# Kernel optimization log

Measured on AMD Instinct MI355X. Metric: run time of the kernel, lower is better.

The kernel has to match this reference:

```python
import jax, jax.numpy as jnp
import numpy as np

T, B, OBS, H, ACT = 256, 1024, 256, 256, 64
SLOPE = 0.1


def setup_inputs() -> dict:
    key = jax.random.key(0)
    ks = jax.random.split(key, 20)
    stdv = 1.0 / np.sqrt(H)
    u = lambda k, shape: jax.random.uniform(k, shape, jnp.float32, -stdv, stdv)
    return {
        "x": jax.random.normal(ks[0], (T, B, OBS), jnp.float32),
        "noise1": jax.random.uniform(ks[1], (T, B, 1), jnp.float32),
        "noise2": jax.random.uniform(ks[2], (T, B, 1), jnp.float32),
        # FCEncoder: two Linear+ReLU layers
        "We1": u(ks[3], (OBS, H)), "be1": u(ks[4], (H,)),
        "We2": u(ks[5], (H, H)), "be2": u(ks[6], (H,)),
        # cell_1 (bottom): U_11 [bottom,4H+1], U_21 [top,4H+1], W_01 [H,4H+1], bias
        "U11_1": u(ks[7], (H, 4 * H + 1)), "U21_1": u(ks[8], (H, 4 * H + 1)),
        "W01_1": u(ks[9], (H, 4 * H + 1)), "b1": u(ks[10], (4 * H + 1,)),
        # cell_2 (top, last layer): no U_21
        "U11_2": u(ks[11], (H, 4 * H + 1)), "W01_2": u(ks[12], (H, 4 * H + 1)),
        "b2": u(ks[13], (4 * H + 1,)),
        "Wh": u(ks[14], (H, H)), "bh": u(ks[15], (H,)),
        "Wp": u(ks[16], (H, ACT)), "bp": u(ks[17], (ACT,)),
    }


def _trigger_train(z_hat, noise):
    # forward: (noise < z_hat).float(); backward: 0.1 * identity (straight-through)
    hard = (noise < z_hat).astype(z_hat.dtype)
    return jax.lax.stop_gradient(hard) + 0.1 * (z_hat - jax.lax.stop_gradient(z_hat))


def _gates(f_s):
    f = jax.nn.sigmoid(f_s[:, 0:H])
    i = jax.nn.sigmoid(f_s[:, H:2 * H])
    o = jax.nn.sigmoid(f_s[:, 2 * H:3 * H])
    g = jnp.tanh(f_s[:, 3 * H:4 * H])
    z_hat = jnp.clip((SLOPE * f_s[:, 4 * H:4 * H + 1] + 1.0) / 2.0, 0.05, 0.95)
    return f, i, o, g, z_hat


def reference(x, noise1, noise2, We1, be1, We2, be2,
              U11_1, U21_1, W01_1, b1, U11_2, W01_2, b2, Wh, bh, Wp, bp):
    # encoder over all timesteps at once (parallel_wrapper equivalent)
    xe = jax.nn.relu(jnp.einsum('tbi,ih->tbh', x, We1) + be1)
    xe = jax.nn.relu(jnp.einsum('tbi,ih->tbh', xe, We2) + be2)

    def step(carry, inp):
        h1, c1, z1, h2, c2 = carry
        xt, n1, n2 = inp
        # ---- cell 1 (not last layer; z_bottom = 1) ----
        fs1 = h1 @ W01_1 + z1 * (h2 @ U21_1) + xt @ U11_1 + b1
        f, i, o, g, zhat1 = _gates(fs1)
        c1n = f * c1 + i * g              # z_bottom == 1 everywhere
        h1n = o * jnp.tanh(c1n)
        z1n = _trigger_train(zhat1, n1)
        # ---- cell 2 (last layer; z_bottom = z1n, s_topdown = 0) ----
        fs2 = h2 @ W01_2 + z1n * (h1n @ U11_2) + b2
        f2, i2, o2, g2, zhat2 = _gates(fs2)
        c2n = (1.0 - z1n) * c2 + z1n * (f2 * c2 + i2 * g2)
        h2n = o2 * jnp.tanh(c2n)
        _ = _trigger_train(zhat2, n2)
        return (h1n, c1n, z1n, h2n, c2n), h2n

    zeros = jnp.zeros((B, H), jnp.float32)
    init = (zeros, zeros, jnp.ones((B, 1), jnp.float32), zeros, zeros)
    _, emb = jax.lax.scan(step, init, (xe, noise1, noise2))  # emb: [T,B,H]

    hid = jax.nn.relu(jnp.einsum('tbh,hk->tbk', emb, Wh) + bh)
    pred = jnp.tanh(jnp.einsum('tbh,ha->tba', hid, Wp) + bp)
    return pred
```

## Files before the change

### kernel.cpp

```cpp
#include <hip/hip_runtime.h>
#include <math.h>

typedef __attribute__((ext_vector_type(8))) _Float16 half8;
typedef __attribute__((ext_vector_type(4))) float    f32x4;
typedef unsigned long long u64;

#define NSTEP 256
#define CH    32
#define NCHUNK (NSTEP/CH)
#define NB    1024
#define HID   256
#define BH    262144
#define LK    40
#define LK1   776
#define LW2   520
#define INV2K 4.8828125e-4f

#define W1H_OFF 0
#define W1L_OFF 49664
#define W2H_OFF 99328
#define WZ_OFF  132608
#define PAN_OFF 135680
#define SEQ_SMEM 135936

__device__ __forceinline__ float sigf(float x){ return 1.f/(1.f+expf(-x)); }
__device__ __forceinline__ void splitf(float v, _Float16& h, _Float16& l){
    h = (_Float16)v; l = (_Float16)((v - (float)h)*2048.f);
}

__global__ __launch_bounds__(256)
void wsplit_k(const float* __restrict__ s0, const float* __restrict__ s1,
              const float* __restrict__ s2, int K, int N, int ldn,
              int kb1, int kb2, int perm,
              _Float16* __restrict__ oh, _Float16* __restrict__ ol)
{
    int idx = blockIdx.x*256 + threadIdx.x;
    if (idx >= N*K) return;
    int n = idx / K, k = idx - n*K;
    int jsrc = perm ? ((n&3)*256 + (n>>2)) : n;
    const float* s = (k < kb1) ? &s0[(size_t)k*ldn]
                   : (k < kb2) ? &s1[(size_t)(k-kb1)*ldn]
                               : &s2[(size_t)(k-kb2)*ldn];
    float v = s[jsrc];
    _Float16 h, l; splitf(v, h, l);
    oh[idx] = h; ol[idx] = l;
}

__global__ void wz_k(const float* __restrict__ W01, const float* __restrict__ U21,
                     const float* __restrict__ U11, float* __restrict__ wz)
{
    int k = blockIdx.x*256 + threadIdx.x;
    if (k >= 768) return;
    wz[k] = (k < 256) ? W01[(size_t)k*1025 + 1024]
          : (k < 512) ? U21[(size_t)(k-256)*1025 + 1024]
                      : U11[(size_t)(k-512)*1025 + 1024];
}

__global__ __launch_bounds__(256)
void init_k(_Float16* h1H, _Float16* h1L, _Float16* h2H, _Float16* h2L,
            float* c1g, float* c2g, unsigned* zcb)
{
    int i = blockIdx.x*256 + threadIdx.x;
    h1H[i] = (_Float16)0.f; h1L[i] = (_Float16)0.f;
    h2H[i] = (_Float16)0.f; h2L[i] = (_Float16)0.f;
    c1g[i] = 0.f; c2g[i] = 0.f;
    if (i < NB) zcb[i] = 1u;
}

template<int AIN, int AOUT, int NCOL>
__global__ __launch_bounds__(256)
void gemm_t(const float* __restrict__ Af,
            const _Float16* __restrict__ Ah_, const _Float16* __restrict__ Al_,
            const _Float16* __restrict__ Bh_, const _Float16* __restrict__ Bl_,
            const float* __restrict__ bias,
            _Float16* __restrict__ Oh, _Float16* __restrict__ Ol,
            float* __restrict__ Of)
{
    constexpr int NT = 8;
    __shared__ __align__(16) char smem[40960];

    const int tid  = threadIdx.x;
    const size_t R0 = (size_t)blockIdx.x*64;
    const int C0   = blockIdx.y*64;
    const int rh   = (tid>>6)&1, ch = tid>>7;
    const int lane = tid&63, lr = lane&15, kq = (lane>>4)<<3;
    const int arow = tid>>2, seg = tid&3;
    const size_t abase = (R0+arow)*256 + seg*8;
    const size_t wbase = (size_t)(C0 + (tid>>2))*256 + seg*8;

    f32x4 am[2][2], ax[2][2];
#pragma unroll
    for (int r=0;r<2;++r)
#pragma unroll
        for (int c=0;c<2;++c){ am[r][c]=(f32x4)0.f; ax[r][c]=(f32x4)0.f; }

    half8 rah, ral, rwh, rwl;
    auto load_tile = [&](int k0, half8& ah, half8& al, half8& wh, half8& wl) {
        if (AIN == 0) {
            float4 a0 = *(const float4*)(Af + abase + k0);
            float4 a1 = *(const float4*)(Af + abase + k0 + 4);
            float av[8] = {a0.x,a0.y,a0.z,a0.w,a1.x,a1.y,a1.z,a1.w};
#pragma unroll
            for (int i=0;i<8;++i){ _Float16 h,l; splitf(av[i],h,l); ah[i]=h; al[i]=l; }
        } else {
            ah = *(const half8*)(Ah_ + abase + k0);
            al = *(const half8*)(Al_ + abase + k0);
        }
        wh = *(const half8*)(Bh_ + wbase + k0);
        wl = *(const half8*)(Bl_ + wbase + k0);
    };
    auto store_tile = [&](int buf) {
        char* bs = smem + buf*20480;
        *(half8*)((_Float16*)(bs        ) + arow*LK + seg*8) = rah;
        *(half8*)((_Float16*)(bs +  5120) + arow*LK + seg*8) = ral;
        *(half8*)((_Float16*)(bs + 10240) + (tid>>2)*LK + seg*8) = rwh;
        *(half8*)((_Float16*)(bs + 15360) + (tid>>2)*LK + seg*8) = rwl;
    };

    load_tile(0, rah, ral, rwh, rwl);
    store_tile(0);

#pragma unroll 2
    for (int kb = 0; kb < NT; ++kb) {
        const int buf = kb & 1;
        half8 nah, nal, nwh, nwl;
        if (kb+1 < NT) load_tile((kb+1)*32, nah, nal, nwh, nwl);
        __syncthreads();
        const char* bs = smem + buf*20480;
        const _Float16* LAh = (const _Float16*)bs;
        const _Float16* LAl = (const _Float16*)(bs +  5120);
        const _Float16* LBh = (const _Float16*)(bs + 10240);
        const _Float16* LBl = (const _Float16*)(bs + 15360);
        half8 fah[2], fal[2], fbh[2], fbl[2];
#pragma unroll
        for (int rf=0;rf<2;++rf) {
            fah[rf] = *(const half8*)(LAh + (rh*32+rf*16+lr)*LK + kq);
            fal[rf] = *(const half8*)(LAl + (rh*32+rf*16+lr)*LK + kq);
        }
#pragma unroll
        for (int cf=0;cf<2;++cf) {
            fbh[cf] = *(const half8*)(LBh + (ch*32+cf*16+lr)*LK + kq);
            fbl[cf] = *(const half8*)(LBl + (ch*32+cf*16+lr)*LK + kq);
        }
#pragma unroll
        for (int cf=0;cf<2;++cf)
#pragma unroll
            for (int rf=0;rf<2;++rf) {
                am[rf][cf] = __builtin_amdgcn_mfma_f32_16x16x32_f16(fah[rf], fbh[cf], am[rf][cf],0,0,0);
                ax[rf][cf] = __builtin_amdgcn_mfma_f32_16x16x32_f16(fah[rf], fbl[cf], ax[rf][cf],0,0,0);
                ax[rf][cf] = __builtin_amdgcn_mfma_f32_16x16x32_f16(fal[rf], fbh[cf], ax[rf][cf],0,0,0);
            }
        if (kb+1 < NT) {
            rah=nah; ral=nal; rwh=nwh; rwl=nwl;
            store_tile((kb+1)&1);
        }
    }

#pragma unroll
    for (int cf=0;cf<2;++cf) {
        int col = C0 + ch*32 + cf*16 + lr;
        float bcol = bias[col];
#pragma unroll
        for (int rf=0;rf<2;++rf)
#pragma unroll
            for (int q=0;q<4;++q) {
                size_t row = R0 + rh*32 + rf*16 + ((lane>>4)<<2) + q;
                float v = am[rf][cf][q] + ax[rf][cf][q]*INV2K + bcol;
                if (AOUT == 0) {
                    v = fmaxf(v, 0.f);
                    _Float16 h,l; splitf(v,h,l);
                    Oh[row*NCOL + col] = h;
                    Ol[row*NCOL + col] = l;
                } else {
                    Of[row*NCOL + col] = tanhf(v);
                }
            }
    }
}

struct PArgs {
    const _Float16 *XeH, *XeL;
    _Float16 *EmH, *EmL;
    const _Float16 *W1h, *W1l, *W2h, *W2l;
    const float *b1, *b2, *wz, *noise;
    _Float16 *h1rH, *h1rL, *h2rH, *h2rL;
    unsigned *zcb;
    float *c1g, *c2g;
    unsigned *ctr;
    unsigned *tick;
    int chunk;
};

__device__ __forceinline__ void barrier_arrive(unsigned* c, int tid)
{
    __syncthreads();
    if (tid == 0)
        __hip_atomic_fetch_add(c, 1u, __ATOMIC_RELAXED, __HIP_MEMORY_SCOPE_AGENT);
}
__device__ __forceinline__ void barrier_wait(unsigned* c, int tid)
{
    if (tid == 0) {
        int guard = 0;
        while (__hip_atomic_load(c, __ATOMIC_RELAXED, __HIP_MEMORY_SCOPE_AGENT) < 32u
               && guard < (1<<17)) {
            __builtin_amdgcn_s_sleep(1);
            ++guard;
        }
    }
    __syncthreads();
}

__global__ __launch_bounds__(512, 1)
void hm_pers_k(PArgs a)
{
    extern __shared__ __align__(16) char smem[];

    const int tid = threadIdx.x, wv = tid>>6, lane = tid&63;
    const int lr = lane&15, hq = lane>>4, kg8 = hq<<3;

    unsigned* pan_sh = (unsigned*)(smem + PAN_OFF);
    if (tid == 0) {
        unsigned xcc;
        asm volatile("s_getreg_b32 %0, hwreg(HW_REG_XCC_ID)" : "=s"(xcc));
        xcc &= 7u;
        unsigned slot = __hip_atomic_fetch_add(a.tick + a.chunk*8 + xcc, 1u,
                          __ATOMIC_RELAXED, __HIP_MEMORY_SCOPE_AGENT);
        pan_sh[0] = xcc;
        pan_sh[1] = slot & 31u;
    }
    __syncthreads();
    const int panel = pan_sh[0], cs = pan_sh[1];
    const int R0 = panel*128, hb = cs*8;
    const int row = R0 + wv*16 + lr;
    const size_t rbase = (size_t)row*HID;
    const int hc0 = hb + hq, hc1 = hb + 4 + hq;

    float b1v[2][4], b2v[2][4];
#pragma unroll
    for (int cf=0; cf<2; ++cf)
#pragma unroll
        for (int q=0;q<4;++q) {
            int hc = hb + cf*4 + hq;
            b1v[cf][q] = a.b1[q*256 + hc];
            b2v[cf][q] = a.b2[q*256 + hc];
        }
    const float b1z = a.b1[1024];

#pragma unroll
    for (int it = 0; it < 12; ++it) {
        int idx = it*512 + tid;
        int hl  = idx >= 3072;
        int e   = idx - hl*3072;
        int c   = e / 96;
        int ks  = e - c*96;
        const _Float16* src = (hl ? a.W1l : a.W1h)
            + (size_t)(cs*32 + c)*768 + ks*8;
        *(half8*)(smem + (hl ? W1L_OFF : W1H_OFF) + (c*LK1 + ks*8)*2)
            = *(const half8*)src;
    }
#pragma unroll
    for (int it = 0; it < 4; ++it) {
        int idx = it*512 + tid;
        int c   = idx >> 6;
        int ks  = idx & 63;
        const _Float16* src = a.W2h + (size_t)(cs*32 + c)*512 + ks*8;
        *(half8*)(smem + W2H_OFF + (c*LW2 + ks*8)*2) = *(const half8*)src;
    }
    {
        float* wzl = (float*)(smem + WZ_OFF);
        for (int i = tid; i < 768; i += 512) wzl[i] = a.wz[i];
    }
    __syncthreads();
    const float* wzl = (const float*)(smem + WZ_OFF);

    float c1s[2] = { a.c1g[rbase + hc0], a.c1g[rbase + hc1] };
    float c2s[2] = { a.c2g[rbase + hc0], a.c2g[rbase + hc1] };
    bool zrv = a.zcb[row] != 0u;

    const _Float16* w2lp[2] = {
        a.W2l + (size_t)(cs*32      + lr)*512 + kg8,
        a.W2l + (size_t)(cs*32 + 16 + lr)*512 + kg8
    };

    half8 pf_h[4], pf_l[4];
    half8 xf_h[8], xf_l[8];
    {
        const _Float16* xeh0 = a.XeH + (size_t)(a.chunk*CH)*BH;
        const _Float16* xel0 = a.XeL + (size_t)(a.chunk*CH)*BH;
#pragma unroll
        for (int kt = 0; kt < 4; ++kt) {
            pf_h[kt] = *(const half8*)(a.h1rH + rbase + kt*32 + kg8);
            pf_l[kt] = *(const half8*)(a.h1rL + rbase + kt*32 + kg8);
        }
#pragma unroll
        for (int j = 0; j < 8; ++j) {
            xf_h[j] = *(const half8*)(xeh0 + rbase + j*32 + kg8);
            xf_l[j] = *(const half8*)(xel0 + rbase + j*32 + kg8);
        }
    }

#pragma unroll 1
    for (int s = 0; s < CH; ++s) {
        const int t = a.chunk*CH + s;
        const _Float16* h1cH = a.h1rH + (size_t)s*BH;
        const _Float16* h1cL = a.h1rL + (size_t)s*BH;
        _Float16*       h1nH = a.h1rH + (size_t)(s+1)*BH;
        _Float16*       h1nL = a.h1rL + (size_t)(s+1)*BH;
        const _Float16* h2cH = a.h2rH + (size_t)s*BH;
        const _Float16* h2cL = a.h2rL + (size_t)s*BH;
        _Float16*       h2nH = a.h2rH + (size_t)(s+1)*BH;
        _Float16*       h2nL = a.h2rL + (size_t)(s+1)*BH;

        auto ld1 = [&](int kt, half8& h, half8& l){
            const int k0 = kt*32;
            if (k0 < 256) { h = *(const half8*)(h1cH + rbase + k0 + kg8);
                            l = *(const half8*)(h1cL + rbase + k0 + kg8); }
            else          { h = *(const half8*)(h2cH + rbase + (k0-256) + kg8);
                            l = *(const half8*)(h2cL + rbase + (k0-256) + kg8); }
        };
        auto ld2 = [&](int kt, half8& h, half8& l){
            const int k0 = kt*32;
            if (k0 < 256) { h = *(const half8*)(h2cH + rbase + k0 + kg8);
                            l = *(const half8*)(h2cL + rbase + k0 + kg8); }
            else          { h = *(const half8*)(h1nH + rbase + (k0-256) + kg8);
                            l = *(const half8*)(h1nL + rbase + (k0-256) + kg8); }
        };

        f32x4 am[2], ax[2];
        am[0]=(f32x4)0.f; am[1]=(f32x4)0.f; ax[0]=(f32x4)0.f; ax[1]=(f32x4)0.f;
        float zacc = 0.f;

#pragma unroll
        for (int kt = 0; kt < 24; ++kt) {
            half8 sh, sl;
            if (kt < 16) { sh = pf_h[kt&3]; sl = pf_l[kt&3]; }
            else         { sh = xf_h[kt-16]; sl = xf_l[kt-16]; }
            if (kt+4 < 16) ld1(kt+4, pf_h[kt&3], pf_l[kt&3]);
            if (kt >= 8 && kt < 16 && !zrv) { sh = half8{}; sl = half8{}; }
#pragma unroll
            for (int i = 0; i < 8; ++i)
                zacc = fmaf((float)sh[i] + (float)sl[i]*INV2K,
                            wzl[kt*32 + kg8 + i], zacc);
#pragma unroll
            for (int cf = 0; cf < 2; ++cf) {
                const int wb = (cf*16 + lr)*LK1 + kt*32 + kg8;
                half8 wh = *(const half8*)((const _Float16*)(smem + W1H_OFF) + wb);
                half8 wl = *(const half8*)((const _Float16*)(smem + W1L_OFF) + wb);
                am[cf] = __builtin_amdgcn_mfma_f32_16x16x32_f16(wh, sh, am[cf],0,0,0);
                ax[cf] = __builtin_amdgcn_mfma_f32_16x16x32_f16(wl, sh, ax[cf],0,0,0);
                ax[cf] = __builtin_amdgcn_mfma_f32_16x16x32_f16(wh, sl, ax[cf],0,0,0);
            }
        }
        zacc += __shfl_xor(zacc, 16);
        zacc += __shfl_xor(zacc, 32);

        float fsz = zacc + b1z;
        float zh = fminf(fmaxf((0.1f*fsz + 1.f)*0.5f, 0.05f), 0.95f);
        const bool znv = a.noise[(size_t)t*NB + row] < zh;

#pragma unroll
        for (int cf = 0; cf < 2; ++cf) {
            float v0 = am[cf][0] + ax[cf][0]*INV2K + b1v[cf][0];
            float v1 = am[cf][1] + ax[cf][1]*INV2K + b1v[cf][1];
            float v2 = am[cf][2] + ax[cf][2]*INV2K + b1v[cf][2];
            float v3 = am[cf][3] + ax[cf][3]*INV2K + b1v[cf][3];
            float f = sigf(v0), i = sigf(v1), o = sigf(v2), g = tanhf(v3);
            float cn = f*c1s[cf] + i*g;
            c1s[cf] = cn;
            float hn = o*tanhf(cn);
            _Float16 hh, hl; splitf(hn, hh, hl);
            const int hc = (cf==0) ? hc0 : hc1;
            h1nH[rbase + hc] = hh; h1nL[rbase + hc] = hl;
            if (s == CH-1) { a.h1rH[rbase + hc] = hh; a.h1rL[rbase + hc] = hl; }
        }
        if (s == CH-1 && hq == 0) a.zcb[row] = znv ? 1u : 0u;

        unsigned* b1c = a.ctr + ((size_t)(a.chunk*CH + s)*2 + 0)*8 + panel;
        barrier_arrive(b1c, tid);

        am[0]=(f32x4)0.f; am[1]=(f32x4)0.f; ax[0]=(f32x4)0.f; ax[1]=(f32x4)0.f;
#pragma unroll
        for (int kt = 0; kt < 4; ++kt) ld2(kt, pf_h[kt], pf_l[kt]);
#pragma unroll
        for (int kt = 0; kt < 8; ++kt) {
            half8 sh = pf_h[kt&3], sl = pf_l[kt&3];
            if (kt+4 < 8) ld2(kt+4, pf_h[kt&3], pf_l[kt&3]);
#pragma unroll
            for (int cf = 0; cf < 2; ++cf) {
                const int wb = (cf*16 + lr)*LW2 + kt*32 + kg8;
                half8 wh = *(const half8*)((const _Float16*)(smem + W2H_OFF) + wb);
                half8 wl = *(const half8*)(w2lp[cf] + kt*32);
                am[cf] = __builtin_amdgcn_mfma_f32_16x16x32_f16(wh, sh, am[cf],0,0,0);
                ax[cf] = __builtin_amdgcn_mfma_f32_16x16x32_f16(wl, sh, ax[cf],0,0,0);
                ax[cf] = __builtin_amdgcn_mfma_f32_16x16x32_f16(wh, sl, ax[cf],0,0,0);
            }
        }
        barrier_wait(b1c, tid);

#pragma unroll
        for (int kt = 8; kt < 12; ++kt) ld2(kt, pf_h[kt&3], pf_l[kt&3]);
#pragma unroll
        for (int kt = 8; kt < 16; ++kt) {
            half8 sh = pf_h[kt&3], sl = pf_l[kt&3];
            if (kt+4 < 16) ld2(kt+4, pf_h[kt&3], pf_l[kt&3]);
            if (!znv) { sh = half8{}; sl = half8{}; }
#pragma unroll
            for (int cf = 0; cf < 2; ++cf) {
                const int wb = (cf*16 + lr)*LW2 + kt*32 + kg8;
                half8 wh = *(const half8*)((const _Float16*)(smem + W2H_OFF) + wb);
                half8 wl = *(const half8*)(w2lp[cf] + kt*32);
                am[cf] = __builtin_amdgcn_mfma_f32_16x16x32_f16(wh, sh, am[cf],0,0,0);
                ax[cf] = __builtin_amdgcn_mfma_f32_16x16x32_f16(wl, sh, ax[cf],0,0,0);
                ax[cf] = __builtin_amdgcn_mfma_f32_16x16x32_f16(wh, sl, ax[cf],0,0,0);
            }
        }

#pragma unroll
        for (int cf = 0; cf < 2; ++cf) {
            float v0 = am[cf][0] + ax[cf][0]*INV2K + b2v[cf][0];
            float v1 = am[cf][1] + ax[cf][1]*INV2K + b2v[cf][1];
            float v2 = am[cf][2] + ax[cf][2]*INV2K + b2v[cf][2];
            float v3 = am[cf][3] + ax[cf][3]*INV2K + b2v[cf][3];
            float f = sigf(v0), i = sigf(v1), o = sigf(v2), g = tanhf(v3);
            float cn = znv ? (f*c2s[cf] + i*g) : c2s[cf];
            c2s[cf] = cn;
            float hn = o*tanhf(cn);
            _Float16 hh, hl; splitf(hn, hh, hl);
            const int hc = (cf==0) ? hc0 : hc1;
            h2nH[rbase + hc] = hh; h2nL[rbase + hc] = hl;
            a.EmH[(size_t)t*BH + rbase + hc] = hh;
            a.EmL[(size_t)t*BH + rbase + hc] = hl;
            if (s == CH-1) { a.h2rH[rbase + hc] = hh; a.h2rL[rbase + hc] = hl; }
        }
        zrv = znv;

        unsigned* b2c = a.ctr + ((size_t)(a.chunk*CH + s)*2 + 1)*8 + panel;
        barrier_arrive(b2c, tid);
        if (s+1 < CH) {
            const _Float16* xehn = a.XeH + (size_t)(t+1)*BH;
            const _Float16* xeln = a.XeL + (size_t)(t+1)*BH;
#pragma unroll
            for (int kt = 0; kt < 4; ++kt) {
                pf_h[kt] = *(const half8*)(h1nH + rbase + kt*32 + kg8);
                pf_l[kt] = *(const half8*)(h1nL + rbase + kt*32 + kg8);
            }
#pragma unroll
            for (int j = 0; j < 8; ++j) {
                xf_h[j] = *(const half8*)(xehn + rbase + j*32 + kg8);
                xf_l[j] = *(const half8*)(xeln + rbase + j*32 + kg8);
            }
        }
        barrier_wait(b2c, tid);
    }

    a.c1g[rbase + hc0] = c1s[0]; a.c1g[rbase + hc1] = c1s[1];
    a.c2g[rbase + hc0] = c2s[0]; a.c2g[rbase + hc1] = c2s[1];
}

extern "C" void kernel_launch(void* const* d_in, const int* in_sizes, int n_in,
                              void* d_out, int out_size, void* d_ws, size_t ws_size,
                              hipStream_t stream)
{
    const float* x     = (const float*)d_in[0];
    const float* n1    = (const float*)d_in[1];
    const float* We1   = (const float*)d_in[3];
    const float* be1   = (const float*)d_in[4];
    const float* We2   = (const float*)d_in[5];
    const float* be2   = (const float*)d_in[6];
    const float* U11_1 = (const float*)d_in[7];
    const float* U21_1 = (const float*)d_in[8];
    const float* W01_1 = (const float*)d_in[9];
    const float* b1    = (const float*)d_in[10];
    const float* U11_2 = (const float*)d_in[11];
    const float* W01_2 = (const float*)d_in[12];
    const float* b2    = (const float*)d_in[13];
    const float* Wh    = (const float*)d_in[14];
    const float* bh    = (const float*)d_in[15];
    const float* Wp    = (const float*)d_in[16];
    const float* bp_   = (const float*)d_in[17];
    float* out = (float*)d_out;

    char* p = (char*)d_ws;
    auto alloc = [&](size_t bytes){ char* q = p; p += (bytes + 255) & ~(size_t)255; return q; };
    _Float16* XeH  = (_Float16*)alloc((size_t)NSTEP*BH*2);
    _Float16* XeL  = (_Float16*)alloc((size_t)NSTEP*BH*2);
    _Float16* EmH  = (_Float16*)alloc((size_t)NSTEP*BH*2);
    _Float16* EmL  = (_Float16*)alloc((size_t)NSTEP*BH*2);
    _Float16* Wt1h = (_Float16*)alloc((size_t)1024*768*2);
    _Float16* Wt1l = (_Float16*)alloc((size_t)1024*768*2);
    _Float16* Wt2h = (_Float16*)alloc((size_t)1024*512*2);
    _Float16* Wt2l = (_Float16*)alloc((size_t)1024*512*2);
    _Float16* We1h = (_Float16*)alloc(256*256*2);
    _Float16* We1l = (_Float16*)alloc(256*256*2);
    _Float16* We2h = (_Float16*)alloc(256*256*2);
    _Float16* We2l = (_Float16*)alloc(256*256*2);
    _Float16* Whh  = (_Float16*)alloc(256*256*2);
    _Float16* Whl  = (_Float16*)alloc(256*256*2);
    _Float16* Wph  = (_Float16*)alloc(64*256*2);
    _Float16* Wpl  = (_Float16*)alloc(64*256*2);
    float*    wz1  = (float*)alloc(768*4);
    _Float16* h1rH = (_Float16*)alloc((size_t)(CH+1)*BH*2);
    _Float16* h1rL = (_Float16*)alloc((size_t)(CH+1)*BH*2);
    _Float16* h2rH = (_Float16*)alloc((size_t)(CH+1)*BH*2);
    _Float16* h2rL = (_Float16*)alloc((size_t)(CH+1)*BH*2);
    unsigned* zcb  = (unsigned*)alloc(NB*4);
    float*    c1g  = (float*)alloc((size_t)BH*4);
    float*    c2g  = (float*)alloc((size_t)BH*4);
    unsigned* ctr  = (unsigned*)alloc((size_t)NCHUNK*CH*2*8*4);
    unsigned* tick = (unsigned*)alloc((size_t)NCHUNK*8*4);
    if (ws_size < (size_t)(p - (char*)d_ws)) return;

    _Float16* TmpH = EmH; _Float16* TmpL = EmL;
    _Float16* TpH  = XeH; _Float16* TpL  = XeL;

    wsplit_k<<<dim3(3072), 256, 0, stream>>>(W01_1, U21_1, U11_1, 768, 1024, 1025, 256, 512, 1, Wt1h, Wt1l);
    wsplit_k<<<dim3(2048), 256, 0, stream>>>(W01_2, U11_2, nullptr, 512, 1024, 1025, 256, 512, 1, Wt2h, Wt2l);
    wsplit_k<<<dim3(256),  256, 0, stream>>>(We1, nullptr, nullptr, 256, 256, 256, 256, 256, 0, We1h, We1l);
    wsplit_k<<<dim3(256),  256, 0, stream>>>(We2, nullptr, nullptr, 256, 256, 256, 256, 256, 0, We2h, We2l);
    wsplit_k<<<dim3(256),  256, 0, stream>>>(Wh,  nullptr, nullptr, 256, 256, 256, 256, 256, 0, Whh,  Whl);
    wsplit_k<<<dim3(64),   256, 0, stream>>>(Wp,  nullptr, nullptr, 256, 64, 64, 256, 256, 0, Wph, Wpl);
    wz_k<<<dim3(3), 256, 0, stream>>>(W01_1, U21_1, U11_1, wz1);
    init_k<<<dim3(1024), 256, 0, stream>>>(h1rH, h1rL, h2rH, h2rL, c1g, c2g, zcb);
    (void)hipMemsetAsync(ctr, 0, (size_t)NCHUNK*CH*2*8*4, stream);
    (void)hipMemsetAsync(tick, 0, (size_t)NCHUNK*8*4, stream);

    for (int c = 0; c < 8; ++c) {
        size_t ro = (size_t)c*32*BH;
        gemm_t<0,0,256><<<dim3(512,4), 256, 0, stream>>>(
            x + ro, nullptr, nullptr, We1h, We1l, be1, TmpH, TmpL, nullptr);
        gemm_t<1,0,256><<<dim3(512,4), 256, 0, stream>>>(
            nullptr, TmpH, TmpL, We2h, We2l, be2, XeH + ro, XeL + ro, nullptr);
    }

    (void)hipFuncSetAttribute((const void*)hm_pers_k,
        hipFuncAttributeMaxDynamicSharedMemorySize, SEQ_SMEM);
    PArgs pa;
    pa.XeH = XeH; pa.XeL = XeL; pa.EmH = EmH; pa.EmL = EmL;
    pa.W1h = Wt1h; pa.W1l = Wt1l; pa.W2h = Wt2h; pa.W2l = Wt2l;
    pa.b1 = b1; pa.b2 = b2; pa.wz = wz1; pa.noise = n1;
    pa.h1rH = h1rH; pa.h1rL = h1rL; pa.h2rH = h2rH; pa.h2rL = h2rL;
    pa.zcb = zcb; pa.c1g = c1g; pa.c2g = c2g; pa.ctr = ctr; pa.tick = tick;
    for (int c = 0; c < NCHUNK; ++c) {
        pa.chunk = c;
        void* kargs[] = { (void*)&pa };
        (void)hipLaunchCooperativeKernel((const void*)hm_pers_k, dim3(256), dim3(512),
                                         kargs, SEQ_SMEM, stream);
    }

    for (int c = 0; c < 8; ++c) {
        size_t ro = (size_t)c*32*BH;
        gemm_t<1,0,256><<<dim3(512,4), 256, 0, stream>>>(
            nullptr, EmH + ro, EmL + ro, Whh, Whl, bh, TpH, TpL, nullptr);
        gemm_t<1,1,64><<<dim3(512,1), 256, 0, stream>>>(
            nullptr, TpH, TpL, Wph, Wpl, bp_, nullptr, nullptr,
            out + (size_t)c*32*NB*64);
    }
}
```

Before: 8.432 ms.

## Overlap cell-1 h1 contribution before the step barrier wait in persistent recurrence

Measured after the change: 8.221 ms. -2.5%, faster.

```diff
diff --git a/kernel.cpp b/kernel.cpp
--- a/kernel.cpp
+++ b/kernel.cpp
@@ -207,7 +207,9 @@
             ++guard;
         }
     }
-    __syncthreads();
+    asm volatile("" ::: "memory");
+    __builtin_amdgcn_s_barrier();
+    asm volatile("" ::: "memory");
 }
 
 __global__ __launch_bounds__(512, 1)
@@ -284,14 +286,40 @@
 
     half8 pf_h[4], pf_l[4];
     half8 xf_h[8], xf_l[8];
+    f32x4 am1[2], ax1[2];
+    float zacc;
+
     {
-        const _Float16* xeh0 = a.XeH + (size_t)(a.chunk*CH)*BH;
-        const _Float16* xel0 = a.XeL + (size_t)(a.chunk*CH)*BH;
+        am1[0]=(f32x4)0.f; am1[1]=(f32x4)0.f;
+        ax1[0]=(f32x4)0.f; ax1[1]=(f32x4)0.f; zacc = 0.f;
 #pragma unroll
         for (int kt = 0; kt < 4; ++kt) {
             pf_h[kt] = *(const half8*)(a.h1rH + rbase + kt*32 + kg8);
             pf_l[kt] = *(const half8*)(a.h1rL + rbase + kt*32 + kg8);
         }
+#pragma unroll
+        for (int kt = 0; kt < 8; ++kt) {
+            half8 sh = pf_h[kt&3], sl = pf_l[kt&3];
+            if (kt+4 < 8) {
+                pf_h[kt&3] = *(const half8*)(a.h1rH + rbase + (kt+4)*32 + kg8);
+                pf_l[kt&3] = *(const half8*)(a.h1rL + rbase + (kt+4)*32 + kg8);
+            }
+#pragma unroll
+            for (int i = 0; i < 8; ++i)
+                zacc = fmaf((float)sh[i] + (float)sl[i]*INV2K,
+                            wzl[kt*32 + kg8 + i], zacc);
+#pragma unroll
+            for (int cf = 0; cf < 2; ++cf) {
+                const int wb = (cf*16 + lr)*LK1 + kt*32 + kg8;
+                half8 wh = *(const half8*)((const _Float16*)(smem + W1H_OFF) + wb);
+                half8 wl = *(const half8*)((const _Float16*)(smem + W1L_OFF) + wb);
+                am1[cf] = __builtin_amdgcn_mfma_f32_16x16x32_f16(wh, sh, am1[cf],0,0,0);
+                ax1[cf] = __builtin_amdgcn_mfma_f32_16x16x32_f16(wl, sh, ax1[cf],0,0,0);
+                ax1[cf] = __builtin_amdgcn_mfma_f32_16x16x32_f16(wh, sl, ax1[cf],0,0,0);
+            }
+        }
+        const _Float16* xeh0 = a.XeH + (size_t)(a.chunk*CH)*BH;
+        const _Float16* xel0 = a.XeL + (size_t)(a.chunk*CH)*BH;
 #pragma unroll
         for (int j = 0; j < 8; ++j) {
             xf_h[j] = *(const half8*)(xeh0 + rbase + j*32 + kg8);
@@ -311,12 +339,10 @@
         _Float16*       h2nH = a.h2rH + (size_t)(s+1)*BH;
         _Float16*       h2nL = a.h2rL + (size_t)(s+1)*BH;
 
-        auto ld1 = [&](int kt, half8& h, half8& l){
+        auto ld1b = [&](int kt, half8& h, half8& l){
             const int k0 = kt*32;
-            if (k0 < 256) { h = *(const half8*)(h1cH + rbase + k0 + kg8);
-                            l = *(const half8*)(h1cL + rbase + k0 + kg8); }
-            else          { h = *(const half8*)(h2cH + rbase + (k0-256) + kg8);
-                            l = *(const half8*)(h2cL + rbase + (k0-256) + kg8); }
+            h = *(const half8*)(h2cH + rbase + (k0-256) + kg8);
+            l = *(const half8*)(h2cL + rbase + (k0-256) + kg8);
         };
         auto ld2 = [&](int kt, half8& h, half8& l){
             const int k0 = kt*32;
@@ -326,17 +352,21 @@
                             l = *(const half8*)(h1nL + rbase + (k0-256) + kg8); }
         };
 
-        f32x4 am[2], ax[2];
-        am[0]=(f32x4)0.f; am[1]=(f32x4)0.f; ax[0]=(f32x4)0.f; ax[1]=(f32x4)0.f;
-        float zacc = 0.f;
-
-#pragma unroll
-        for (int kt = 0; kt < 24; ++kt) {
+        if (s > 0)
+            barrier_wait(a.ctr + ((size_t)(a.chunk*CH + s-1)*2 + 1)*8 + panel, tid);
+
+#pragma unroll
+        for (int kt = 8; kt < 12; ++kt) ld1b(kt, pf_h[kt&3], pf_l[kt&3]);
+#pragma unroll
+        for (int kt = 8; kt < 24; ++kt) {
             half8 sh, sl;
-            if (kt < 16) { sh = pf_h[kt&3]; sl = pf_l[kt&3]; }
-            else         { sh = xf_h[kt-16]; sl = xf_l[kt-16]; }
-            if (kt+4 < 16) ld1(kt+4, pf_h[kt&3], pf_l[kt&3]);
-            if (kt >= 8 && kt < 16 && !zrv) { sh = half8{}; sl = half8{}; }
+            if (kt < 16) {
+                sh = pf_h[kt&3]; sl = pf_l[kt&3];
+                if (kt+4 < 16) ld1b(kt+4, pf_h[kt&3], pf_l[kt&3]);
+                if (!zrv) { sh = half8{}; sl = half8{}; }
+            } else {
+                sh = xf_h[kt-16]; sl = xf_l[kt-16];
+            }
 #pragma unroll
             for (int i = 0; i < 8; ++i)
                 zacc = fmaf((float)sh[i] + (float)sl[i]*INV2K,
@@ -346,9 +376,9 @@
                 const int wb = (cf*16 + lr)*LK1 + kt*32 + kg8;
                 half8 wh = *(const half8*)((const _Float16*)(smem + W1H_OFF) + wb);
                 half8 wl = *(const half8*)((const _Float16*)(smem + W1L_OFF) + wb);
-                am[cf] = __builtin_amdgcn_mfma_f32_16x16x32_f16(wh, sh, am[cf],0,0,0);
-                ax[cf] = __builtin_amdgcn_mfma_f32_16x16x32_f16(wl, sh, ax[cf],0,0,0);
-                ax[cf] = __builtin_amdgcn_mfma_f32_16x16x32_f16(wh, sl, ax[cf],0,0,0);
+                am1[cf] = __builtin_amdgcn_mfma_f32_16x16x32_f16(wh, sh, am1[cf],0,0,0);
+                ax1[cf] = __builtin_amdgcn_mfma_f32_16x16x32_f16(wl, sh, ax1[cf],0,0,0);
+                ax1[cf] = __builtin_amdgcn_mfma_f32_16x16x32_f16(wh, sl, ax1[cf],0,0,0);
             }
         }
         zacc += __shfl_xor(zacc, 16);
@@ -360,10 +390,10 @@
 
 #pragma unroll
         for (int cf = 0; cf < 2; ++cf) {
-            float v0 = am[cf][0] + ax[cf][0]*INV2K + b1v[cf][0];
-            float v1 = am[cf][1] + ax[cf][1]*INV2K + b1v[cf][1];
-            float v2 = am[cf][2] + ax[cf][2]*INV2K + b1v[cf][2];
-            float v3 = am[cf][3] + ax[cf][3]*INV2K + b1v[cf][3];
+            float v0 = am1[cf][0] + ax1[cf][0]*INV2K + b1v[cf][0];
+            float v1 = am1[cf][1] + ax1[cf][1]*INV2K + b1v[cf][1];
+            float v2 = am1[cf][2] + ax1[cf][2]*INV2K + b1v[cf][2];
+            float v3 = am1[cf][3] + ax1[cf][3]*INV2K + b1v[cf][3];
             float f = sigf(v0), i = sigf(v1), o = sigf(v2), g = tanhf(v3);
             float cn = f*c1s[cf] + i*g;
             c1s[cf] = cn;
@@ -378,7 +408,9 @@
         unsigned* b1c = a.ctr + ((size_t)(a.chunk*CH + s)*2 + 0)*8 + panel;
         barrier_arrive(b1c, tid);
 
-        am[0]=(f32x4)0.f; am[1]=(f32x4)0.f; ax[0]=(f32x4)0.f; ax[1]=(f32x4)0.f;
+        f32x4 am2[2], ax2[2];
+        am2[0]=(f32x4)0.f; am2[1]=(f32x4)0.f;
+        ax2[0]=(f32x4)0.f; ax2[1]=(f32x4)0.f;
 #pragma unroll
         for (int kt = 0; kt < 4; ++kt) ld2(kt, pf_h[kt], pf_l[kt]);
 #pragma unroll
@@ -390,9 +422,9 @@
                 const int wb = (cf*16 + lr)*LW2 + kt*32 + kg8;
                 half8 wh = *(const half8*)((const _Float16*)(smem + W2H_OFF) + wb);
                 half8 wl = *(const half8*)(w2lp[cf] + kt*32);
-                am[cf] = __builtin_amdgcn_mfma_f32_16x16x32_f16(wh, sh, am[cf],0,0,0);
-                ax[cf] = __builtin_amdgcn_mfma_f32_16x16x32_f16(wl, sh, ax[cf],0,0,0);
-                ax[cf] = __builtin_amdgcn_mfma_f32_16x16x32_f16(wh, sl, ax[cf],0,0,0);
+                am2[cf] = __builtin_amdgcn_mfma_f32_16x16x32_f16(wh, sh, am2[cf],0,0,0);
+                ax2[cf] = __builtin_amdgcn_mfma_f32_16x16x32_f16(wl, sh, ax2[cf],0,0,0);
+                ax2[cf] = __builtin_amdgcn_mfma_f32_16x16x32_f16(wh, sl, ax2[cf],0,0,0);
             }
         }
         barrier_wait(b1c, tid);
@@ -409,18 +441,18 @@
                 const int wb = (cf*16 + lr)*LW2 + kt*32 + kg8;
                 half8 wh = *(const half8*)((const _Float16*)(smem + W2H_OFF) + wb);
                 half8 wl = *(const half8*)(w2lp[cf] + kt*32);
-                am[cf] = __builtin_amdgcn_mfma_f32_16x16x32_f16(wh, sh, am[cf],0,0,0);
-                ax[cf] = __builtin_amdgcn_mfma_f32_16x16x32_f16(wl, sh, ax[cf],0,0,0);
-                ax[cf] = __builtin_amdgcn_mfma_f32_16x16x32_f16(wh, sl, ax[cf],0,0,0);
+                am2[cf] = __builtin_amdgcn_mfma_f32_16x16x32_f16(wh, sh, am2[cf],0,0,0);
+                ax2[cf] = __builtin_amdgcn_mfma_f32_16x16x32_f16(wl, sh, ax2[cf],0,0,0);
+                ax2[cf] = __builtin_amdgcn_mfma_f32_16x16x32_f16(wh, sl, ax2[cf],0,0,0);
             }
         }
 
 #pragma unroll
         for (int cf = 0; cf < 2; ++cf) {
-            float v0 = am[cf][0] + ax[cf][0]*INV2K + b2v[cf][0];
-            float v1 = am[cf][1] + ax[cf][1]*INV2K + b2v[cf][1];
-            float v2 = am[cf][2] + ax[cf][2]*INV2K + b2v[cf][2];
-            float v3 = am[cf][3] + ax[cf][3]*INV2K + b2v[cf][3];
+            float v0 = am2[cf][0] + ax2[cf][0]*INV2K + b2v[cf][0];
+            float v1 = am2[cf][1] + ax2[cf][1]*INV2K + b2v[cf][1];
+            float v2 = am2[cf][2] + ax2[cf][2]*INV2K + b2v[cf][2];
+            float v3 = am2[cf][3] + ax2[cf][3]*INV2K + b2v[cf][3];
             float f = sigf(v0), i = sigf(v1), o = sigf(v2), g = tanhf(v3);
             float cn = znv ? (f*c2s[cf] + i*g) : c2s[cf];
             c2s[cf] = cn;
@@ -436,21 +468,44 @@
 
         unsigned* b2c = a.ctr + ((size_t)(a.chunk*CH + s)*2 + 1)*8 + panel;
         barrier_arrive(b2c, tid);
+
         if (s+1 < CH) {
-            const _Float16* xehn = a.XeH + (size_t)(t+1)*BH;
-            const _Float16* xeln = a.XeL + (size_t)(t+1)*BH;
+            am1[0]=(f32x4)0.f; am1[1]=(f32x4)0.f;
+            ax1[0]=(f32x4)0.f; ax1[1]=(f32x4)0.f; zacc = 0.f;
 #pragma unroll
             for (int kt = 0; kt < 4; ++kt) {
                 pf_h[kt] = *(const half8*)(h1nH + rbase + kt*32 + kg8);
                 pf_l[kt] = *(const half8*)(h1nL + rbase + kt*32 + kg8);
             }
 #pragma unroll
+            for (int kt = 0; kt < 8; ++kt) {
+                half8 sh = pf_h[kt&3], sl = pf_l[kt&3];
+                if (kt+4 < 8) {
+                    pf_h[kt&3] = *(const half8*)(h1nH + rbase + (kt+4)*32 + kg8);
+                    pf_l[kt&3] = *(const half8*)(h1nL + rbase + (kt+4)*32 + kg8);
+                }
+#pragma unroll
+                for (int i = 0; i < 8; ++i)
+                    zacc = fmaf((float)sh[i] + (float)sl[i]*INV2K,
+                                wzl[kt*32 + kg8 + i], zacc);
+#pragma unroll
+                for (int cf = 0; cf < 2; ++cf) {
+                    const int wb = (cf*16 + lr)*LK1 + kt*32 + kg8;
+                    half8 wh = *(const half8*)((const _Float16*)(smem + W1H_OFF) + wb);
+                    half8 wl = *(const half8*)((const _Float16*)(smem + W1L_OFF) + wb);
+                    am1[cf] = __builtin_amdgcn_mfma_f32_16x16x32_f16(wh, sh, am1[cf],0,0,0);
+                    ax1[cf] = __builtin_amdgcn_mfma_f32_16x16x32_f16(wl, sh, ax1[cf],0,0,0);
+                    ax1[cf] = __builtin_amdgcn_mfma_f32_16x16x32_f16(wh, sl, ax1[cf],0,0,0);
+                }
+            }
+            const _Float16* xehn = a.XeH + (size_t)(t+1)*BH;
+            const _Float16* xeln = a.XeL + (size_t)(t+1)*BH;
+#pragma unroll
             for (int j = 0; j < 8; ++j) {
                 xf_h[j] = *(const half8*)(xehn + rbase + j*32 + kg8);
                 xf_l[j] = *(const half8*)(xeln + rbase + j*32 + kg8);
             }
         }
-        barrier_wait(b2c, tid);
     }
 
     a.c1g[rbase + hc0] = c1s[0]; a.c1g[rbase + hc1] = c1s[1];
@@ -542,9 +597,7 @@
     pa.zcb = zcb; pa.c1g = c1g; pa.c2g = c2g; pa.ctr = ctr; pa.tick = tick;
     for (int c = 0; c < NCHUNK; ++c) {
         pa.chunk = c;
-        void* kargs[] = { (void*)&pa };
-        (void)hipLaunchCooperativeKernel((const void*)hm_pers_k, dim3(256), dim3(512),
-                                         kargs, SEQ_SMEM, stream);
+        hm_pers_k<<<dim3(256), dim3(512), SEQ_SMEM, stream>>>(pa);
     }
 
     for (int c = 0; c < 8; ++c) {
```
